# Kernel optimization log

Measured on AMD Instinct MI355X. Metric: run time of the kernel, lower is better.

Reference implementation:

```python
import jax, jax.numpy as jnp
import numpy as np

N_HEADS = 8
CHUNK = 512


def _mha(x, Wq, Wk, Wv, Wo, n_heads):
    # Standard no-bias multi-head self-attention; torch Linear => x @ W.T
    B, T, d = x.shape
    hd = d // n_heads
    q = (x @ Wq.T).reshape(B, T, n_heads, hd)
    k = (x @ Wk.T).reshape(B, T, n_heads, hd)
    v = (x @ Wv.T).reshape(B, T, n_heads, hd)
    scores = jnp.einsum('bqhd,bkhd->bhqk', q, k) / jnp.sqrt(jnp.asarray(hd, x.dtype))
    attn = jax.nn.softmax(scores, axis=-1)
    out = jnp.einsum('bhqk,bkhd->bqhd', attn, v).reshape(B, T, d)
    return out @ Wo.T


def _cross_chunk_attn(s, n_heads):
    # SDPA over chunk summaries with q=k=v=s (no projections inside)
    B, nc, d = s.shape
    hd = d // n_heads
    q = s.reshape(B, nc, n_heads, hd)
    scores = jnp.einsum('bqhd,bkhd->bhqk', q, q) / jnp.sqrt(jnp.asarray(hd, s.dtype))
    attn = jax.nn.softmax(scores, axis=-1)
    out = jnp.einsum('bhqk,bkhd->bqhd', attn, q).reshape(B, nc, d)
    return out


def setup_inputs() -> dict:
    key = jax.random.key(0)
    ks = jax.random.split(key, 6)
    B, T, d = 2, 16384, 512
    scale = 1.0 / np.sqrt(d)
    x = jax.random.normal(ks[0], (B, T, d), dtype=jnp.float32)
    Wq = jax.random.normal(ks[1], (d, d), dtype=jnp.float32) * scale
    Wk = jax.random.normal(ks[2], (d, d), dtype=jnp.float32) * scale
    Wv = jax.random.normal(ks[3], (d, d), dtype=jnp.float32) * scale
    Wo = jax.random.normal(ks[4], (d, d), dtype=jnp.float32) * scale
    Wg = jax.random.normal(ks[5], (d, d), dtype=jnp.float32) * scale
    return {'x': x, 'Wq': Wq, 'Wk': Wk, 'Wv': Wv, 'Wo': Wo, 'Wg': Wg}


def reference(x, Wq, Wk, Wv, Wo, Wg):
    B, T, d = x.shape
    pad = (CHUNK - T % CHUNK) % CHUNK
    if pad > 0:
        x = jnp.pad(x, ((0, 0), (0, pad), (0, 0)))
    T_padded = T + pad
    n_chunks = T_padded // CHUNK
    # 1) chunk: (B*n_chunks, CHUNK, d)
    chunked = x.reshape(B * n_chunks, CHUNK, d)
    # 2) local attention within each chunk
    local_out = _mha(chunked, Wq, Wk, Wv, Wo, N_HEADS)
    # 3) mean-pool summaries -> (B, n_chunks, d)
    summaries = local_out.mean(axis=1).reshape(B, n_chunks, d)
    # 4) global projection + cross-chunk SDPA
    global_ctx = _cross_chunk_attn(summaries @ Wg.T, N_HEADS)
    # 5) broadcast chunk context back to tokens
    enriched = local_out + global_ctx.reshape(B * n_chunks, 1, d)
    # 6) recombine and trim padding
    out = enriched.reshape(B, T_padded, d)
    if pad > 0:
        out = out[:, :T, :]
    return out
```

## Files before the change

### kernel.cpp

```cpp
#include <hip/hip_runtime.h>

typedef __attribute__((ext_vector_type(8))) short short8;
typedef __attribute__((ext_vector_type(4))) float f32x4;
typedef __attribute__((ext_vector_type(16))) float f32x16;

#define DEV static __device__ __forceinline__

DEV float bf2f(unsigned short u) {
  union { unsigned int u32; float f; } v; v.u32 = ((unsigned int)u) << 16; return v.f;
}
DEV unsigned short f2bf(float f) {
  union { float f; unsigned int u; } v; v.f = f;
  unsigned int r = v.u + 0x7fffu + ((v.u >> 16) & 1u);
  return (unsigned short)(r >> 16);
}
DEV unsigned cvtpk(float lo, float hi) {
  unsigned r;
  asm("v_cvt_pk_bf16_f32 %0, %1, %2" : "=v"(r) : "v"(lo), "v"(hi));
  return r;
}
DEV void plswap(unsigned &a, unsigned &b) {
  asm("v_permlane32_swap_b32 %0, %1" : "+v"(a), "+v"(b));
}
DEV short8 mk8(unsigned a, unsigned b, unsigned c, unsigned d) {
  union { unsigned u[4]; short8 v; } x;
  x.u[0] = a; x.u[1] = b; x.u[2] = c; x.u[3] = d; return x.v;
}

#define GLL16(g, l) __builtin_amdgcn_global_load_lds( \
    (const __attribute__((address_space(1))) void*)(g), \
    (__attribute__((address_space(3))) void*)(l), 16, 0, 0)

constexpr int D  = 512;
constexpr int BT = 32768;

__global__ __launch_bounds__(256) void k_convert(
    const float* __restrict__ x, const float* __restrict__ Wq, const float* __restrict__ Wk,
    const float* __restrict__ Wv, const float* __restrict__ Wo,
    unsigned short* __restrict__ xb, unsigned short* __restrict__ wqkv,
    unsigned short* __restrict__ wo_b) {
  int idx = blockIdx.x * 256 + threadIdx.x;
  const int NX4 = (BT * D) / 4;
  const float* src; unsigned short* dst; size_t i4;
  if (idx < NX4) {
    src = x; dst = xb; i4 = (size_t)idx * 4;
  } else {
    int t = idx - NX4;
    int w = t >> 16;
    int within = t & 65535;
    src = (w == 0) ? Wq : (w == 1) ? Wk : (w == 2) ? Wv : Wo;
    dst = (w < 3) ? (wqkv + (size_t)w * D * D) : wo_b;
    i4 = (size_t)within * 4;
  }
  float4 v = *(const float4*)(src + i4);
  ushort4 o; o.x = f2bf(v.x); o.y = f2bf(v.y); o.z = f2bf(v.z); o.w = f2bf(v.w);
  *(ushort4*)(dst + i4) = o;
}

template<int NBLK, int EPI>
__global__ __launch_bounds__(512, 4) void k_gemm(
    const unsigned short* __restrict__ A, const unsigned short* __restrict__ Bm,
    unsigned short* __restrict__ O0, unsigned short* __restrict__ O1,
    unsigned short* __restrict__ O2) {
  __shared__ unsigned short Ash[3][128 * 32];
  __shared__ unsigned short Bsh[3][256 * 32];
  const int tid = threadIdx.x;
  const int lane = tid & 63, w = tid >> 6;
  const int lr = lane & 15, lg = lane >> 4;
  const int cpx = gridDim.x >> 3;
  const int bid = blockIdx.x;
  const int work = (bid & 7) * cpx + (bid >> 3);
  const int nb = work % NBLK, mb = work / NBLK;
  const int m0 = mb * 128, n0 = nb * 256;
  const int wr = w >> 2, wc = w & 3;

  const int sr = lane >> 2;
  const int sg8 = ((lane & 3) ^ ((lane >> 3) & 3)) * 8;
  const unsigned short* gA  = A  + (size_t)(m0 + w * 16 + sr) * D + sg8;
  const unsigned short* gB0 = Bm + (size_t)(n0 + w * 16 + sr) * D + sg8;
  const unsigned short* gB1 = Bm + (size_t)(n0 + 128 + w * 16 + sr) * D + sg8;

  auto stage = [&](int kt, int b) {
    GLL16(gA  + kt * 32, &Ash[b][w * 512]);
    GLL16(gB0 + kt * 32, &Bsh[b][w * 512]);
    GLL16(gB1 + kt * 32, &Bsh[b][(128 + w * 16) * 32]);
  };

  f32x4 acc[4][4];
  #pragma unroll
  for (int m = 0; m < 4; ++m)
    #pragma unroll
    for (int n = 0; n < 4; ++n) acc[m][n] = (f32x4){0.f, 0.f, 0.f, 0.f};

  stage(0, 0);
  stage(1, 1);

  const int rdsw = (lg ^ ((lr >> 1) & 3)) * 8;

#define GSTEP(KT, WN) { \
    asm volatile("s_waitcnt vmcnt(" #WN ")" ::: "memory"); \
    __builtin_amdgcn_s_barrier(); \
    if ((KT) + 2 < 16) stage((KT) + 2, ((KT) + 2) % 3); \
    const unsigned short* Ac = Ash[(KT) % 3]; \
    const unsigned short* Bc = Bsh[(KT) % 3]; \
    short8 af[4], bf[4]; \
    _Pragma("unroll") \
    for (int m = 0; m < 4; ++m) \
      af[m] = *(const short8*)&Ac[(wr * 64 + m * 16 + lr) * 32 + rdsw]; \
    _Pragma("unroll") \
    for (int n = 0; n < 4; ++n) \
      bf[n] = *(const short8*)&Bc[(wc * 64 + n * 16 + lr) * 32 + rdsw]; \
    __builtin_amdgcn_s_setprio(1); \
    _Pragma("unroll") \
    for (int m = 0; m < 4; ++m) \
      _Pragma("unroll") \
      for (int n = 0; n < 4; ++n) \
        acc[m][n] = __builtin_amdgcn_mfma_f32_16x16x32_bf16(af[m], bf[n], acc[m][n], 0, 0, 0); \
    __builtin_amdgcn_s_setprio(0); \
  }

  GSTEP(0, 3)  GSTEP(1, 3)  GSTEP(2, 3)  GSTEP(3, 3)
  GSTEP(4, 3)  GSTEP(5, 3)  GSTEP(6, 3)  GSTEP(7, 3)
  GSTEP(8, 3)  GSTEP(9, 3)  GSTEP(10, 3) GSTEP(11, 3)
  GSTEP(12, 3) GSTEP(13, 3) GSTEP(14, 3) GSTEP(15, 0)
#undef GSTEP

  if (EPI == 1 && nb >= 4) {
    #pragma unroll
    for (int m = 0; m < 4; ++m) {
      #pragma unroll
      for (int n = 0; n < 4; ++n) {
        int e = (n0 - 1024) + wc * 64 + n * 16 + lr;
        int grow = m0 + wr * 64 + m * 16 + lg * 4;
        int bc = grow >> 9, key = grow & 511;
        ushort4 pk;
        pk.x = f2bf(acc[m][n][0]); pk.y = f2bf(acc[m][n][1]);
        pk.z = f2bf(acc[m][n][2]); pk.w = f2bf(acc[m][n][3]);
        *(ushort4*)&O2[(size_t)(bc * 512 + e) * 512 + key] = pk;
      }
    }
  } else {
    unsigned short* Od = O0;
    int cshift = 0;
    if (EPI == 1 && nb >= 2) { Od = O1; cshift = 512; }
    #pragma unroll
    for (int m = 0; m < 4; ++m) {
      #pragma unroll
      for (int n = 0; n < 4; ++n) {
        int col = n0 + wc * 64 + n * 16 + lr - cshift;
        #pragma unroll
        for (int r = 0; r < 4; ++r) {
          int row = m0 + wr * 64 + m * 16 + lg * 4 + r;
          Od[(size_t)row * D + col] = f2bf(acc[m][n][r]);
        }
      }
    }
  }
}

__global__ __launch_bounds__(512, 4) void k_attn(
    const unsigned short* __restrict__ Q, const unsigned short* __restrict__ K,
    const unsigned short* __restrict__ Vt, unsigned short* __restrict__ attn_out) {
  __shared__ char lds[3][16384];
  const int tid = threadIdx.x;
  const int lane = tid & 63, w = tid >> 6;
  const int l31 = lane & 31, hl = lane >> 5;
  int work = ((blockIdx.x & 7) << 7) + (blockIdx.x >> 3);
  int qh = work & 1, h = (work >> 1) & 7, bc = work >> 4;
  int qbase = bc * 512 + qh * 256 + w * 32;

  short8 qf[4];
  {
    const unsigned short* qp = Q + (size_t)(qbase + l31) * D + h * 64 + hl * 8;
    #pragma unroll
    for (int ks = 0; ks < 4; ++ks) qf[ks] = *(const short8*)(qp + ks * 16);
  }

  const int srow  = w * 8 + (lane >> 3);
  const int sslot = (lane & 7) ^ ((lane >> 3) & 7);
  const unsigned short* gK = K  + (size_t)(bc * 512 + srow) * D + h * 64 + sslot * 8;
  const unsigned short* gV = Vt + (size_t)(bc * 512 + h * 64 + srow) * D + sslot * 8;
  auto STAGE = [&](int T, int B) {
    GLL16(gK + (size_t)(T) * 64 * D, &lds[B][w * 1024]);
    GLL16(gV + (T) * 64,             &lds[B][8192 + w * 1024]);
  };

  f32x16 oA, oB;
  #pragma unroll
  for (int i = 0; i < 16; ++i) { oA[i] = 0.f; oB[i] = 0.f; }
  float mrun = -3e38f, lrun = 0.f;
  const float scale = 0.125f;
  const int x7 = l31 & 7;

  STAGE(0, 0);
  STAGE(1, 1);

  #pragma unroll
  for (int t = 0; t < 8; ++t) {
    if (t == 0 || t == 7) asm volatile("s_waitcnt vmcnt(0)" ::: "memory");
    else                  asm volatile("s_waitcnt vmcnt(2)" ::: "memory");
    __builtin_amdgcn_s_barrier();
    if (t < 6) STAGE(t + 2, (t + 2) % 3);
    const char* kb = lds[t % 3];
    const char* vb = lds[t % 3] + 8192;

    f32x16 sA, sB;
    #pragma unroll
    for (int i = 0; i < 16; ++i) { sA[i] = 0.f; sB[i] = 0.f; }
    #pragma unroll
    for (int ks = 0; ks < 4; ++ks) {
      int sl = ((ks * 2 + hl) ^ x7) * 16;
      short8 kf0 = *(const short8*)(kb + l31 * 128 + sl);
      short8 kf1 = *(const short8*)(kb + (32 + l31) * 128 + sl);
      sA = __builtin_amdgcn_mfma_f32_32x32x16_bf16(kf0, qf[ks], sA, 0, 0, 0);
      sB = __builtin_amdgcn_mfma_f32_32x32x16_bf16(kf1, qf[ks], sB, 0, 0, 0);
    }

    float pm = sA[0];
    #pragma unroll
    for (int i = 1; i < 16; ++i) pm = fmaxf(pm, sA[i]);
    #pragma unroll
    for (int i = 0; i < 16; ++i) pm = fmaxf(pm, sB[i]);
    pm = fmaxf(pm, __shfl_xor(pm, 32));
    float mnew = fmaxf(mrun, pm);
    float alpha = __expf((mrun - mnew) * scale);
    float ls = 0.f;
    #pragma unroll
    for (int i = 0; i < 16; ++i) { float p = __expf((sA[i] - mnew) * scale); sA[i] = p; ls += p; }
    #pragma unroll
    for (int i = 0; i < 16; ++i) { float p = __expf((sB[i] - mnew) * scale); sB[i] = p; ls += p; }
    ls += __shfl_xor(ls, 32);
    lrun = lrun * alpha + ls;
    mrun = mnew;
    #pragma unroll
    for (int i = 0; i < 16; ++i) { oA[i] *= alpha; oB[i] *= alpha; }

    unsigned dA[8], dB[8];
    #pragma unroll
    for (int i = 0; i < 8; ++i) {
      dA[i] = cvtpk(sA[2 * i], sA[2 * i + 1]);
      dB[i] = cvtpk(sB[2 * i], sB[2 * i + 1]);
    }
    plswap(dA[0], dA[2]); plswap(dA[1], dA[3]);
    plswap(dA[4], dA[6]); plswap(dA[5], dA[7]);
    plswap(dB[0], dB[2]); plswap(dB[1], dB[3]);
    plswap(dB[4], dB[6]); plswap(dB[5], dB[7]);
    short8 pf[4] = { mk8(dA[0], dA[1], dA[2], dA[3]), mk8(dA[4], dA[5], dA[6], dA[7]),
                     mk8(dB[0], dB[1], dB[2], dB[3]), mk8(dB[4], dB[5], dB[6], dB[7]) };

    #pragma unroll
    for (int k4 = 0; k4 < 4; ++k4) {
      int sl = ((k4 * 2 + hl) ^ x7) * 16;
      short8 vf0 = *(const short8*)(vb + l31 * 128 + sl);
      short8 vf1 = *(const short8*)(vb + (32 + l31) * 128 + sl);
      oA = __builtin_amdgcn_mfma_f32_32x32x16_bf16(vf0, pf[k4], oA, 0, 0, 0);
      oB = __builtin_amdgcn_mfma_f32_32x32x16_bf16(vf1, pf[k4], oB, 0, 0, 0);
    }
  }

  __syncthreads();
  float inv = 1.f / lrun;
  char* tr = &lds[0][0] + w * 4096;
  #pragma unroll
  for (int r = 0; r < 16; ++r) {
    int e0 = (r & 3) + 8 * (r >> 2) + 4 * hl;
    *(unsigned short*)(tr + ((l31 * 128 + e0 * 2) ^ (x7 << 4)))        = f2bf(oA[r] * inv);
    *(unsigned short*)(tr + ((l31 * 128 + (32 + e0) * 2) ^ (x7 << 4))) = f2bf(oB[r] * inv);
  }
  unsigned short* op = attn_out + (size_t)(qbase + l31) * D + h * 64 + hl * 32;
  #pragma unroll
  for (int s = 0; s < 4; ++s) {
    int slot = (hl * 4 + s) ^ x7;
    short8 v = *(const short8*)(tr + l31 * 128 + slot * 16);
    *(short8*)(op + s * 8) = v;
  }
}

__global__ __launch_bounds__(256) void k_mean(const unsigned short* __restrict__ lout,
                                              float* __restrict__ summ) {
  int bc = blockIdx.x;
  int col = blockIdx.y * 256 + threadIdx.x;
  const unsigned short* p = lout + (size_t)bc * 512 * 512 + col;
  float s = 0.f;
  #pragma unroll 8
  for (int r = 0; r < 512; ++r) s += bf2f(p[(size_t)r * 512]);
  summ[bc * 512 + col] = s * (1.f / 512.f);
}

__global__ __launch_bounds__(256) void k_sg(const float* __restrict__ summ,
                                            const float* __restrict__ Wg,
                                            float* __restrict__ sg) {
  __shared__ float srow[512];
  int m = blockIdx.x >> 1, half = blockIdx.x & 1;
  for (int i = threadIdx.x; i < 512; i += 256) srow[i] = summ[m * 512 + i];
  __syncthreads();
  int n = half * 256 + threadIdx.x;
  const float* wr = Wg + (size_t)n * 512;
  float s = 0.f;
  #pragma unroll 8
  for (int kk = 0; kk < 512; ++kk) s += srow[kk] * wr[kk];
  sg[m * 512 + n] = s;
}

__global__ __launch_bounds__(256) void k_gattn(const float* __restrict__ sg,
                                               float* __restrict__ gctx) {
  __shared__ float qs[32][64];
  __shared__ float sc[32][32];
  int b = blockIdx.x >> 3, h = blockIdx.x & 7;
  int tid = threadIdx.x;
  for (int i = tid; i < 2048; i += 256) {
    int r = i >> 6, e = i & 63;
    qs[r][e] = sg[(size_t)(b * 32 + r) * 512 + h * 64 + e];
  }
  __syncthreads();
  for (int p = tid; p < 1024; p += 256) {
    int qi = p >> 5, ki = p & 31;
    float s = 0.f;
    #pragma unroll 8
    for (int e = 0; e < 64; ++e) s += qs[qi][e] * qs[ki][e];
    sc[qi][ki] = s * 0.125f;
  }
  __syncthreads();
  if (tid < 32) {
    float mx = -1e30f;
    for (int k2 = 0; k2 < 32; ++k2) mx = fmaxf(mx, sc[tid][k2]);
    float sm = 0.f;
    for (int k2 = 0; k2 < 32; ++k2) { float p = __expf(sc[tid][k2] - mx); sc[tid][k2] = p; sm += p; }
    float iv = 1.f / sm;
    for (int k2 = 0; k2 < 32; ++k2) sc[tid][k2] *= iv;
  }
  __syncthreads();
  for (int i = tid; i < 2048; i += 256) {
    int r = i >> 6, e = i & 63;
    float o = 0.f;
    #pragma unroll 8
    for (int k2 = 0; k2 < 32; ++k2) o += sc[r][k2] * qs[k2][e];
    gctx[(size_t)(b * 32 + r) * 512 + h * 64 + e] = o;
  }
}

__global__ __launch_bounds__(256) void k_final(const unsigned short* __restrict__ lout,
                                               const float* __restrict__ gctx,
                                               float* __restrict__ out) {
  size_t idx = (size_t)blockIdx.x * 256 + threadIdx.x;
  size_t i = idx * 4;
  int c = (int)(i & 511);
  int bcg = (int)(i >> 18);
  ushort4 lv = *(const ushort4*)(lout + i);
  float4 g = *(const float4*)(gctx + (size_t)bcg * 512 + c);
  float4 o;
  o.x = bf2f(lv.x) + g.x;
  o.y = bf2f(lv.y) + g.y;
  o.z = bf2f(lv.z) + g.z;
  o.w = bf2f(lv.w) + g.w;
  *(float4*)(out + i) = o;
}

extern "C" void kernel_launch(void* const* d_in, const int* in_sizes, int n_in,
                              void* d_out, int out_size, void* d_ws, size_t ws_size,
                              hipStream_t stream) {
  const float* x  = (const float*)d_in[0];
  const float* Wq = (const float*)d_in[1];
  const float* Wk = (const float*)d_in[2];
  const float* Wv = (const float*)d_in[3];
  const float* Wo = (const float*)d_in[4];
  const float* Wg = (const float*)d_in[5];
  float* out = (float*)d_out;

  char* ws = (char*)d_ws;
  unsigned short* xb   = (unsigned short*)(ws);
  unsigned short* q    = (unsigned short*)(ws + 33554432);
  unsigned short* kb   = (unsigned short*)(ws + 67108864);
  unsigned short* vt   = (unsigned short*)(ws + 100663296);
  unsigned short* wqkv = (unsigned short*)(ws + 134217728);
  unsigned short* wo_b = (unsigned short*)(ws + 135790592);
  float* summ = (float*)(ws + 136314880);
  float* sgp  = (float*)(ws + 136445952);
  float* gctx = (float*)(ws + 136577024);
  unsigned short* attn_out = xb;
  unsigned short* local_bf = q;

  k_convert<<<17408, 256, 0, stream>>>(x, Wq, Wk, Wv, Wo, xb, wqkv, wo_b);
  k_gemm<6, 1><<<1536, 512, 0, stream>>>(xb, wqkv, q, kb, vt);
  k_attn<<<1024, 512, 0, stream>>>(q, kb, vt, attn_out);
  k_gemm<2, 0><<<512, 512, 0, stream>>>(attn_out, wo_b, local_bf, nullptr, nullptr);
  k_mean<<<dim3(64, 2), 256, 0, stream>>>(local_bf, summ);
  k_sg<<<128, 256, 0, stream>>>(summ, Wg, sgp);
  k_gattn<<<16, 256, 0, stream>>>(sgp, gctx);
  k_final<<<16384, 256, 0, stream>>>(local_bf, gctx, out);
}
```

Baseline: 235.3 us.

## Fold softmax scale into Q projection, use exp2 with lazy rescale, reswizzle LDS

The QKV projection epilogue now multiplies the Q output by scale*log2(e), so the attention kernel can use exp2f directly without a per-element scale multiply. The online softmax skips rescaling the output accumulators unless some lane's new max exceeds the running max by more than 8 in log2 units. The LDS swizzle for K/V tiles changes to a row-plus-warp-dependent XOR pattern meant to reduce bank conflicts. The changes cost extra bf16 rounding of the pre-scaled Q and a wave-wide vote per tile, and they let the exponent arguments grow up to 2^8 before rescaling.

```diff
diff --git a/kernel.cpp b/kernel.cpp
--- a/kernel.cpp
+++ b/kernel.cpp
@@ -142,6 +142,7 @@
   } else {
     unsigned short* Od = O0;
     int cshift = 0;
+    float cs = (EPI == 1 && nb < 2) ? 0.1803368801f : 1.0f;
     if (EPI == 1 && nb >= 2) { Od = O1; cshift = 512; }
     #pragma unroll
     for (int m = 0; m < 4; ++m) {
@@ -151,7 +152,7 @@
         #pragma unroll
         for (int r = 0; r < 4; ++r) {
           int row = m0 + wr * 64 + m * 16 + lg * 4 + r;
-          Od[(size_t)row * D + col] = f2bf(acc[m][n][r]);
+          Od[(size_t)row * D + col] = f2bf(acc[m][n][r] * cs);
         }
       }
     }
@@ -176,10 +177,11 @@
     for (int ks = 0; ks < 4; ++ks) qf[ks] = *(const short8*)(qp + ks * 16);
   }
 
-  const int srow  = w * 8 + (lane >> 3);
-  const int sslot = (lane & 7) ^ ((lane >> 3) & 7);
-  const unsigned short* gK = K  + (size_t)(bc * 512 + srow) * D + h * 64 + sslot * 8;
-  const unsigned short* gV = Vt + (size_t)(bc * 512 + h * 64 + srow) * D + sslot * 8;
+  const int lr3 = lane >> 3;
+  const int srow = w * 8 + lr3;
+  const int sq = (lane & 7) ^ ((lr3 + w) & 7);
+  const unsigned short* gK = K  + (size_t)(bc * 512 + srow) * D + h * 64 + sq * 8;
+  const unsigned short* gV = Vt + (size_t)(bc * 512 + h * 64 + srow) * D + sq * 8;
   auto STAGE = [&](int T, int B) {
     GLL16(gK + (size_t)(T) * 64 * D, &lds[B][w * 1024]);
     GLL16(gV + (T) * 64,             &lds[B][8192 + w * 1024]);
@@ -189,8 +191,8 @@
   #pragma unroll
   for (int i = 0; i < 16; ++i) { oA[i] = 0.f; oB[i] = 0.f; }
   float mrun = -3e38f, lrun = 0.f;
-  const float scale = 0.125f;
-  const int x7 = l31 & 7;
+  const int f0 = (l31 + (l31 >> 3)) & 7;
+  const int f1 = (f0 + 4) & 7;
 
   STAGE(0, 0);
   STAGE(1, 1);
@@ -209,31 +211,34 @@
     for (int i = 0; i < 16; ++i) { sA[i] = 0.f; sB[i] = 0.f; }
     #pragma unroll
     for (int ks = 0; ks < 4; ++ks) {
-      int sl = ((ks * 2 + hl) ^ x7) * 16;
-      short8 kf0 = *(const short8*)(kb + l31 * 128 + sl);
-      short8 kf1 = *(const short8*)(kb + (32 + l31) * 128 + sl);
+      int c = ks * 2 + hl;
+      short8 kf0 = *(const short8*)(kb + l31 * 128 + ((c ^ f0) << 4));
+      short8 kf1 = *(const short8*)(kb + (32 + l31) * 128 + ((c ^ f1) << 4));
       sA = __builtin_amdgcn_mfma_f32_32x32x16_bf16(kf0, qf[ks], sA, 0, 0, 0);
       sB = __builtin_amdgcn_mfma_f32_32x32x16_bf16(kf1, qf[ks], sB, 0, 0, 0);
     }
 
-    float pm = sA[0];
-    #pragma unroll
-    for (int i = 1; i < 16; ++i) pm = fmaxf(pm, sA[i]);
-    #pragma unroll
-    for (int i = 0; i < 16; ++i) pm = fmaxf(pm, sB[i]);
+    float pm = fmaxf(sA[0], sA[1]);
+    #pragma unroll
+    for (int i = 2; i < 16; i += 2) pm = fmaxf(pm, fmaxf(sA[i], sA[i + 1]));
+    #pragma unroll
+    for (int i = 0; i < 16; i += 2) pm = fmaxf(pm, fmaxf(sB[i], sB[i + 1]));
     pm = fmaxf(pm, __shfl_xor(pm, 32));
-    float mnew = fmaxf(mrun, pm);
-    float alpha = __expf((mrun - mnew) * scale);
+    if (!__all(pm - mrun <= 8.f)) {
+      float mnew = fmaxf(mrun, pm);
+      float alpha = exp2f(mrun - mnew);
+      mrun = mnew;
+      lrun *= alpha;
+      #pragma unroll
+      for (int i = 0; i < 16; ++i) { oA[i] *= alpha; oB[i] *= alpha; }
+    }
     float ls = 0.f;
     #pragma unroll
-    for (int i = 0; i < 16; ++i) { float p = __expf((sA[i] - mnew) * scale); sA[i] = p; ls += p; }
-    #pragma unroll
-    for (int i = 0; i < 16; ++i) { float p = __expf((sB[i] - mnew) * scale); sB[i] = p; ls += p; }
+    for (int i = 0; i < 16; ++i) { float p = exp2f(sA[i] - mrun); sA[i] = p; ls += p; }
+    #pragma unroll
+    for (int i = 0; i < 16; ++i) { float p = exp2f(sB[i] - mrun); sB[i] = p; ls += p; }
     ls += __shfl_xor(ls, 32);
-    lrun = lrun * alpha + ls;
-    mrun = mnew;
-    #pragma unroll
-    for (int i = 0; i < 16; ++i) { oA[i] *= alpha; oB[i] *= alpha; }
+    lrun += ls;
 
     unsigned dA[8], dB[8];
     #pragma unroll
@@ -250,9 +255,9 @@
 
     #pragma unroll
     for (int k4 = 0; k4 < 4; ++k4) {
-      int sl = ((k4 * 2 + hl) ^ x7) * 16;
-      short8 vf0 = *(const short8*)(vb + l31 * 128 + sl);
-      short8 vf1 = *(const short8*)(vb + (32 + l31) * 128 + sl);
+      int c = k4 * 2 + hl;
+      short8 vf0 = *(const short8*)(vb + l31 * 128 + ((c ^ f0) << 4));
+      short8 vf1 = *(const short8*)(vb + (32 + l31) * 128 + ((c ^ f1) << 4));
       oA = __builtin_amdgcn_mfma_f32_32x32x16_bf16(vf0, pf[k4], oA, 0, 0, 0);
       oB = __builtin_amdgcn_mfma_f32_32x32x16_bf16(vf1, pf[k4], oB, 0, 0, 0);
     }
@@ -260,6 +265,7 @@
 
   __syncthreads();
   float inv = 1.f / lrun;
+  const int x7 = l31 & 7;
   char* tr = &lds[0][0] + w * 4096;
   #pragma unroll
   for (int r = 0; r < 16; ++r) {
```

Result: slower. 242.1 us (+2.9%).
